# Kernel tuning notes

Measured on AMD Instinct MI355X. Metric: run time of the kernel, lower is better.

## Reference

```python
import jax, jax.numpy as jnp
import numpy as np
from jax import lax

# Static config matching init_kwargs
CIN, COUT, K, STRIDE, PAD = 64, 64, 3, 1, 1
SCALE = 100.0          # scale_factor
MIN_SUMMARY = -512     # static lower bound for the quantized-summary memo table
MEM_SIZE = 1025        # static memo table size (covers summaries in [-512, 512])


def setup_inputs() -> dict:
    key = jax.random.key(0)
    k1, k2, k3 = jax.random.split(key, 3)
    fmap = jax.random.normal(k1, (8, CIN, 112, 112), dtype=jnp.float32)
    weight = jax.random.normal(k2, (COUT, K * K * CIN), dtype=jnp.float32) * 0.05
    bias = jax.random.normal(k3, (COUT,), dtype=jnp.float32) * 0.05
    return {"fmap": fmap, "weight": weight, "bias": bias}


def _unfold(fmap):
    # torch F.unfold(fmap, K, stride, pad).permute(0,2,1): [N, P, K*K*Cin]
    patches = lax.conv_general_dilated_patches(
        fmap, (K, K), (STRIDE, STRIDE), ((PAD, PAD), (PAD, PAD)))  # [N, Cin*K*K, Hout, Wout]
    N, D, Hout, Wout = patches.shape
    return patches.reshape(N, D, Hout * Wout).transpose(0, 2, 1), Hout, Wout


def reference(fmap, weight, bias):
    patches, Hout, Wout = _unfold(fmap)          # [N, P, D]
    N, P, D = patches.shape

    # Quantized avg summary per patch: fmap.mean(dim=2).mul_(scale).int()
    summaries = (patches.mean(axis=2) * SCALE).astype(jnp.int32)  # [N, P]
    bins = jnp.clip(summaries - MIN_SUMMARY, 0, MEM_SIZE - 1)     # [N, P]

    def per_image(p, b):
        # Dedup: each summary bin computed once from its first-occurring patch.
        idx = jnp.arange(P, dtype=jnp.int32)
        first = jnp.full((MEM_SIZE,), P, dtype=jnp.int32).at[b].min(idx)  # scatter-min
        rep_patch = p[first[b]]                   # [P, D] gather of representatives
        return rep_patch @ weight.T + bias        # [P, Cout]

    out = jax.vmap(per_image)(patches, bins)      # [N, P, Cout]
    return out.transpose(0, 2, 1).reshape(N, COUT, Hout, Wout)


if __name__ == "__main__":
    inp = setup_inputs()
    print(reference(**inp).shape)
```

## Files before the change

### kernel.cpp

```cpp
#include <hip/hip_runtime.h>

#define N_IMG 8
#define CIN   64
#define H     112
#define W     112
#define P     (H * W)
#define PG    (P / 4)
#define D     576
#define COUT  64
#define MEM   1025
#define SENT  P

__global__ __launch_bounds__(256) void prep_kernel(
    const float* __restrict__ weight, float* __restrict__ wT,
    int* __restrict__ first) {
  int i = blockIdx.x * 256 + threadIdx.x;
  if (i < N_IMG * MEM) first[i] = SENT;
  if (i < D * COUT) {
    int d = i / COUT, co = i - d * COUT;
    wT[i] = weight[co * D + d];
  }
}

__global__ __launch_bounds__(256) void chan_sum_kernel(
    const float* __restrict__ fmap, double* __restrict__ T) {
  __shared__ double partial[4][64][4];
  int t = threadIdx.x;
  int q = t >> 6, lane = t & 63;
  int n = blockIdx.y;
  int pg = blockIdx.x * 64 + lane;
  int p4 = pg * 4;
  const float* base = fmap + (size_t)n * CIN * P + p4;
  double s0 = 0.0, s1 = 0.0, s2 = 0.0, s3 = 0.0;
  int c0 = q * 16;
  #pragma unroll
  for (int c = c0; c < c0 + 16; ++c) {
    float4 v = *reinterpret_cast<const float4*>(base + (size_t)c * P);
    s0 += (double)v.x; s1 += (double)v.y; s2 += (double)v.z; s3 += (double)v.w;
  }
  partial[q][lane][0] = s0; partial[q][lane][1] = s1;
  partial[q][lane][2] = s2; partial[q][lane][3] = s3;
  __syncthreads();
  if (t < 64) {
    double4 o;
    o.x = partial[0][t][0] + partial[1][t][0] + partial[2][t][0] + partial[3][t][0];
    o.y = partial[0][t][1] + partial[1][t][1] + partial[2][t][1] + partial[3][t][1];
    o.z = partial[0][t][2] + partial[1][t][2] + partial[2][t][2] + partial[3][t][2];
    o.w = partial[0][t][3] + partial[1][t][3] + partial[2][t][3] + partial[3][t][3];
    *reinterpret_cast<double4*>(T + (size_t)n * P + (blockIdx.x * 64 + t) * 4) = o;
  }
}

__global__ __launch_bounds__(1024) void bins_kernel(
    const double* __restrict__ T, int* __restrict__ bins, int* __restrict__ first) {
  __shared__ int lfirst[MEM];
  int t = threadIdx.x;
  for (int i = t; i < MEM; i += 1024) lfirst[i] = SENT;
  __syncthreads();
  int n = blockIdx.y;
  int p = blockIdx.x * 1024 + t;
  if (p < P) {
    int h = p / W, w = p - h * W;
    const double* Tn = T + (size_t)n * P;
    double s = 0.0;
    #pragma unroll
    for (int dh = -1; dh <= 1; ++dh) {
      int hh = h + dh;
      if (hh < 0 || hh >= H) continue;
      #pragma unroll
      for (int dw = -1; dw <= 1; ++dw) {
        int ww = w + dw;
        if (ww < 0 || ww >= W) continue;
        s += Tn[hh * W + ww];
      }
    }
    float sf = (float)s;
    float mean = sf / 576.0f;
    float v = mean * 100.0f;
    int qv = (int)v;
    int b = qv + 512;
    b = b < 0 ? 0 : (b > MEM - 1 ? MEM - 1 : b);
    bins[n * P + p] = b;
    atomicMin(&lfirst[b], p);
  }
  __syncthreads();
  for (int i = t; i < MEM; i += 1024) {
    int v = lfirst[i];
    if (v != SENT) atomicMin(&first[n * MEM + i], v);
  }
}

__global__ __launch_bounds__(256) void rep_kernel(
    const float* __restrict__ fmap, const float* __restrict__ wT,
    const float* __restrict__ bias, const int* __restrict__ first,
    float* __restrict__ rep) {
  int b = blockIdx.x;
  int n = blockIdx.y;
  int fi = first[n * MEM + b];
  if (fi >= SENT) return;
  __shared__ float patch[D];
  __shared__ float partial[4][COUT];
  int t = threadIdx.x;
  int h = fi / W, w = fi - h * W;
  for (int d = t; d < D; d += 256) {
    int c = d / 9, r = d - c * 9;
    int kh = r / 3, kw = r - kh * 3;
    int hh = h + kh - 1, ww = w + kw - 1;
    float val = 0.0f;
    if (hh >= 0 && hh < H && ww >= 0 && ww < W)
      val = fmap[((size_t)(n * CIN + c)) * P + hh * W + ww];
    patch[d] = val;
  }
  __syncthreads();
  int co = t & 63, seg = t >> 6;
  float acc = 0.0f;
  int d0 = seg * 144;
  #pragma unroll 4
  for (int d = d0; d < d0 + 144; ++d)
    acc += patch[d] * wT[d * COUT + co];
  partial[seg][co] = acc;
  __syncthreads();
  if (t < COUT) {
    float total = partial[0][t] + partial[1][t] + partial[2][t] + partial[3][t] + bias[t];
    rep[((size_t)n * MEM + b) * COUT + t] = total;
  }
}

__global__ __launch_bounds__(256) void scatter_kernel(
    const int* __restrict__ bins, const float* __restrict__ rep,
    float* __restrict__ out) {
  int idx = blockIdx.x * blockDim.x + threadIdx.x;
  const int PV = P / 4;
  if (idx >= N_IMG * COUT * PV) return;
  int pv = idx % PV;
  int rest = idx / PV;
  int co = rest & 63;
  int n = rest >> 6;
  int4 b4 = *reinterpret_cast<const int4*>(bins + n * P + pv * 4);
  const float* repn = rep + (size_t)n * MEM * COUT + co;
  float4 o;
  o.x = repn[(size_t)b4.x * COUT];
  o.y = repn[(size_t)b4.y * COUT];
  o.z = repn[(size_t)b4.z * COUT];
  o.w = repn[(size_t)b4.w * COUT];
  *reinterpret_cast<float4*>(out + ((size_t)n * COUT + co) * P + pv * 4) = o;
}

extern "C" void kernel_launch(void* const* d_in, const int* in_sizes, int n_in,
                              void* d_out, int out_size, void* d_ws, size_t ws_size,
                              hipStream_t stream) {
  const float* fmap   = (const float*)d_in[0];
  const float* weight = (const float*)d_in[1];
  const float* bias   = (const float*)d_in[2];
  float* out = (float*)d_out;

  char* ws = (char*)d_ws;
  double* T   = (double*)(ws);
  int*   bins = (int*)  (ws + 802816);
  int*  first = (int*)  (ws + 1204224);
  float*   wT = (float*)(ws + 1237248);
  float*  rep = (float*)(ws + 1384704);

  hipLaunchKernelGGL(prep_kernel, dim3(144), dim3(256), 0, stream,
                     weight, wT, first);
  hipLaunchKernelGGL(chan_sum_kernel, dim3(49, 8), dim3(256), 0, stream,
                     fmap, T);
  hipLaunchKernelGGL(bins_kernel, dim3(13, 8), dim3(1024), 0, stream,
                     T, bins, first);
  hipLaunchKernelGGL(rep_kernel, dim3(MEM, N_IMG), dim3(256), 0, stream,
                     fmap, wT, bias, first, rep);
  hipLaunchKernelGGL(scatter_kernel, dim3((N_IMG * COUT * (P / 4) + 255) / 256), dim3(256), 0, stream,
                     bins, rep, out);
}
```

Baseline: 113.3 us.

## Fuse all stages into one cooperative kernel with grid-wide syncs

```diff
diff --git a/kernel.cpp b/kernel.cpp
--- a/kernel.cpp
+++ b/kernel.cpp
@@ -1,4 +1,7 @@
 #include <hip/hip_runtime.h>
+#include <hip/hip_cooperative_groups.h>
+
+namespace cg = cooperative_groups;
 
 #define N_IMG 8
 #define CIN   64
@@ -10,56 +13,58 @@
 #define COUT  64
 #define MEM   1025
 #define SENT  P
+#define GRID  512
+#define BLK   256
 
-__global__ __launch_bounds__(256) void prep_kernel(
-    const float* __restrict__ weight, float* __restrict__ wT,
-    int* __restrict__ first) {
-  int i = blockIdx.x * 256 + threadIdx.x;
-  if (i < N_IMG * MEM) first[i] = SENT;
-  if (i < D * COUT) {
-    int d = i / COUT, co = i - d * COUT;
-    wT[i] = weight[co * D + d];
+__global__ __launch_bounds__(BLK) void fused_kernel(
+    const float* __restrict__ fmap, const float* __restrict__ weight,
+    const float* __restrict__ bias, float* __restrict__ out,
+    double* __restrict__ T, int* __restrict__ bins, int* __restrict__ first,
+    float* __restrict__ wT, float* __restrict__ rep) {
+  cg::grid_group grid = cg::this_grid();
+  __shared__ union SharedU {
+    int lfirst[MEM];
+    struct { float patch[D]; float partial[4][COUT]; } rp;
+  } sh;
+
+  const int t   = threadIdx.x;
+  const int gid = blockIdx.x;
+  const int tid = gid * BLK + t;
+
+  if (tid < N_IMG * MEM) first[tid] = SENT;
+  if (tid < D * COUT) {
+    int d = tid / COUT, co = tid - d * COUT;
+    wT[tid] = weight[co * D + d];
   }
-}
+  if (tid < N_IMG * PG * 4) {
+    int task = tid >> 2, seg = tid & 3;
+    int n = task / PG;
+    int pg = task - n * PG;
+    const float* base = fmap + ((size_t)n * CIN) * P + pg * 4;
+    double s0 = 0.0, s1 = 0.0, s2 = 0.0, s3 = 0.0;
+    int c0 = seg * 16;
+    #pragma unroll
+    for (int c = c0; c < c0 + 16; ++c) {
+      float4 v = *reinterpret_cast<const float4*>(base + (size_t)c * P);
+      s0 += (double)v.x; s1 += (double)v.y; s2 += (double)v.z; s3 += (double)v.w;
+    }
+    s0 += __shfl_xor(s0, 1); s1 += __shfl_xor(s1, 1);
+    s2 += __shfl_xor(s2, 1); s3 += __shfl_xor(s3, 1);
+    s0 += __shfl_xor(s0, 2); s1 += __shfl_xor(s1, 2);
+    s2 += __shfl_xor(s2, 2); s3 += __shfl_xor(s3, 2);
+    if (seg == 0) {
+      double4 o; o.x = s0; o.y = s1; o.z = s2; o.w = s3;
+      *reinterpret_cast<double4*>(T + (size_t)n * P + pg * 4) = o;
+    }
+  }
 
-__global__ __launch_bounds__(256) void chan_sum_kernel(
-    const float* __restrict__ fmap, double* __restrict__ T) {
-  __shared__ double partial[4][64][4];
-  int t = threadIdx.x;
-  int q = t >> 6, lane = t & 63;
-  int n = blockIdx.y;
-  int pg = blockIdx.x * 64 + lane;
-  int p4 = pg * 4;
-  const float* base = fmap + (size_t)n * CIN * P + p4;
-  double s0 = 0.0, s1 = 0.0, s2 = 0.0, s3 = 0.0;
-  int c0 = q * 16;
-  #pragma unroll
-  for (int c = c0; c < c0 + 16; ++c) {
-    float4 v = *reinterpret_cast<const float4*>(base + (size_t)c * P);
-    s0 += (double)v.x; s1 += (double)v.y; s2 += (double)v.z; s3 += (double)v.w;
-  }
-  partial[q][lane][0] = s0; partial[q][lane][1] = s1;
-  partial[q][lane][2] = s2; partial[q][lane][3] = s3;
-  __syncthreads();
-  if (t < 64) {
-    double4 o;
-    o.x = partial[0][t][0] + partial[1][t][0] + partial[2][t][0] + partial[3][t][0];
-    o.y = partial[0][t][1] + partial[1][t][1] + partial[2][t][1] + partial[3][t][1];
-    o.z = partial[0][t][2] + partial[1][t][2] + partial[2][t][2] + partial[3][t][2];
-    o.w = partial[0][t][3] + partial[1][t][3] + partial[2][t][3] + partial[3][t][3];
-    *reinterpret_cast<double4*>(T + (size_t)n * P + (blockIdx.x * 64 + t) * 4) = o;
-  }
-}
+  grid.sync();
 
-__global__ __launch_bounds__(1024) void bins_kernel(
-    const double* __restrict__ T, int* __restrict__ bins, int* __restrict__ first) {
-  __shared__ int lfirst[MEM];
-  int t = threadIdx.x;
-  for (int i = t; i < MEM; i += 1024) lfirst[i] = SENT;
-  __syncthreads();
-  int n = blockIdx.y;
-  int p = blockIdx.x * 1024 + t;
-  if (p < P) {
+  if (gid < N_IMG * 49) {
+    for (int i = t; i < MEM; i += BLK) sh.lfirst[i] = SENT;
+    __syncthreads();
+    int n = gid / 49;
+    int p = (gid % 49) * BLK + t;
     int h = p / W, w = p - h * W;
     const double* Tn = T + (size_t)n * P;
     double s = 0.0;
@@ -81,69 +86,64 @@
     int b = qv + 512;
     b = b < 0 ? 0 : (b > MEM - 1 ? MEM - 1 : b);
     bins[n * P + p] = b;
-    atomicMin(&lfirst[b], p);
+    atomicMin(&sh.lfirst[b], p);
+    __syncthreads();
+    for (int i = t; i < MEM; i += BLK) {
+      int v2 = sh.lfirst[i];
+      if (v2 != SENT) atomicMin(&first[n * MEM + i], v2);
+    }
   }
-  __syncthreads();
-  for (int i = t; i < MEM; i += 1024) {
-    int v = lfirst[i];
-    if (v != SENT) atomicMin(&first[n * MEM + i], v);
+
+  grid.sync();
+
+  for (int pair = gid; pair < N_IMG * MEM; pair += GRID) {
+    int n = pair / MEM, b = pair - n * MEM;
+    int fi = first[pair];
+    if (fi >= SENT) continue;
+    int h = fi / W, w = fi - h * W;
+    for (int d = t; d < D; d += BLK) {
+      int c = d / 9, r = d - c * 9;
+      int kh = r / 3, kw = r - kh * 3;
+      int hh = h + kh - 1, ww = w + kw - 1;
+      float val = 0.0f;
+      if (hh >= 0 && hh < H && ww >= 0 && ww < W)
+        val = fmap[((size_t)(n * CIN + c)) * P + hh * W + ww];
+      sh.rp.patch[d] = val;
+    }
+    __syncthreads();
+    int co = t & 63, seg = t >> 6;
+    float acc = 0.0f;
+    int d0 = seg * 144;
+    #pragma unroll 4
+    for (int d = d0; d < d0 + 144; ++d)
+      acc += sh.rp.patch[d] * wT[d * COUT + co];
+    sh.rp.partial[seg][co] = acc;
+    __syncthreads();
+    if (t < COUT) {
+      float total = sh.rp.partial[0][t] + sh.rp.partial[1][t] +
+                    sh.rp.partial[2][t] + sh.rp.partial[3][t] + bias[t];
+      rep[((size_t)pair) * COUT + t] = total;
+    }
+    __syncthreads();
   }
-}
 
-__global__ __launch_bounds__(256) void rep_kernel(
-    const float* __restrict__ fmap, const float* __restrict__ wT,
-    const float* __restrict__ bias, const int* __restrict__ first,
-    float* __restrict__ rep) {
-  int b = blockIdx.x;
-  int n = blockIdx.y;
-  int fi = first[n * MEM + b];
-  if (fi >= SENT) return;
-  __shared__ float patch[D];
-  __shared__ float partial[4][COUT];
-  int t = threadIdx.x;
-  int h = fi / W, w = fi - h * W;
-  for (int d = t; d < D; d += 256) {
-    int c = d / 9, r = d - c * 9;
-    int kh = r / 3, kw = r - kh * 3;
-    int hh = h + kh - 1, ww = w + kw - 1;
-    float val = 0.0f;
-    if (hh >= 0 && hh < H && ww >= 0 && ww < W)
-      val = fmap[((size_t)(n * CIN + c)) * P + hh * W + ww];
-    patch[d] = val;
+  grid.sync();
+
+  const int NTASK = N_IMG * COUT * PG;
+  for (int idx = tid; idx < NTASK; idx += GRID * BLK) {
+    int pv = idx % PG;
+    int rest = idx / PG;
+    int co = rest & 63;
+    int n = rest >> 6;
+    int4 b4 = *reinterpret_cast<const int4*>(bins + n * P + pv * 4);
+    const float* repn = rep + (size_t)n * MEM * COUT + co;
+    float4 o;
+    o.x = repn[(size_t)b4.x * COUT];
+    o.y = repn[(size_t)b4.y * COUT];
+    o.z = repn[(size_t)b4.z * COUT];
+    o.w = repn[(size_t)b4.w * COUT];
+    *reinterpret_cast<float4*>(out + ((size_t)n * COUT + co) * P + pv * 4) = o;
   }
-  __syncthreads();
-  int co = t & 63, seg = t >> 6;
-  float acc = 0.0f;
-  int d0 = seg * 144;
-  #pragma unroll 4
-  for (int d = d0; d < d0 + 144; ++d)
-    acc += patch[d] * wT[d * COUT + co];
-  partial[seg][co] = acc;
-  __syncthreads();
-  if (t < COUT) {
-    float total = partial[0][t] + partial[1][t] + partial[2][t] + partial[3][t] + bias[t];
-    rep[((size_t)n * MEM + b) * COUT + t] = total;
-  }
-}
-
-__global__ __launch_bounds__(256) void scatter_kernel(
-    const int* __restrict__ bins, const float* __restrict__ rep,
-    float* __restrict__ out) {
-  int idx = blockIdx.x * blockDim.x + threadIdx.x;
-  const int PV = P / 4;
-  if (idx >= N_IMG * COUT * PV) return;
-  int pv = idx % PV;
-  int rest = idx / PV;
-  int co = rest & 63;
-  int n = rest >> 6;
-  int4 b4 = *reinterpret_cast<const int4*>(bins + n * P + pv * 4);
-  const float* repn = rep + (size_t)n * MEM * COUT + co;
-  float4 o;
-  o.x = repn[(size_t)b4.x * COUT];
-  o.y = repn[(size_t)b4.y * COUT];
-  o.z = repn[(size_t)b4.z * COUT];
-  o.w = repn[(size_t)b4.w * COUT];
-  *reinterpret_cast<float4*>(out + ((size_t)n * COUT + co) * P + pv * 4) = o;
 }
 
 extern "C" void kernel_launch(void* const* d_in, const int* in_sizes, int n_in,
@@ -161,14 +161,8 @@
   float*   wT = (float*)(ws + 1237248);
   float*  rep = (float*)(ws + 1384704);
 
-  hipLaunchKernelGGL(prep_kernel, dim3(144), dim3(256), 0, stream,
-                     weight, wT, first);
-  hipLaunchKernelGGL(chan_sum_kernel, dim3(49, 8), dim3(256), 0, stream,
-                     fmap, T);
-  hipLaunchKernelGGL(bins_kernel, dim3(13, 8), dim3(1024), 0, stream,
-                     T, bins, first);
-  hipLaunchKernelGGL(rep_kernel, dim3(MEM, N_IMG), dim3(256), 0, stream,
-                     fmap, wT, bias, first, rep);
-  hipLaunchKernelGGL(scatter_kernel, dim3((N_IMG * COUT * (P / 4) + 255) / 256), dim3(256), 0, stream,
-                     bins, rep, out);
+  void* args[] = {(void*)&fmap, (void*)&weight, (void*)&bias, (void*)&out,
+                  (void*)&T, (void*)&bins, (void*)&first, (void*)&wT, (void*)&rep};
+  hipLaunchCooperativeKernel((const void*)fused_kernel, dim3(GRID), dim3(BLK),
+                             args, 0, stream);
 }
```

Result: slower. 326.6 us (+188.2%).
